# Kernel tuning notes

Measured on AMD Instinct MI355X. Metric: run time of the kernel, lower is better.

## Reference

```python
import jax, jax.numpy as jnp
import numpy as np


def _pair_indices(field_num):
    # upper-triangular (row < col) pairs, same order as the torch double loop
    r, c = np.triu_indices(field_num, k=1)
    return jnp.asarray(r, dtype=jnp.int32), jnp.asarray(c, dtype=jnp.int32)


def setup_inputs() -> dict:
    key = jax.random.key(0)
    x = jax.random.normal(key, (4096, 39, 64), dtype=jnp.float32)
    return {"x": x}


def reference(x) -> jnp.ndarray:
    # x: (B, F, D). Output: (B, F*(F-1)/2) pairwise inner products.
    field_num = x.shape[1]
    rows, cols = _pair_indices(field_num)  # static: derived from shape
    p = x[:, rows, :]  # (B, P, D) gather of row-field embeddings
    q = x[:, cols, :]  # (B, P, D) gather of col-field embeddings
    return jnp.sum(p * q, axis=2)  # (B, P)
```

## Files before the change

kernel.cpp:

```cpp
#include <hip/hip_runtime.h>


constexpr int NFIELD = 39;
constexpr int DIM    = 64;
constexpr int K4     = DIM / 4;
constexpr int NPAIR  = 741;
constexpr int NROWP  = 40;
constexpr int BPB    = 4;
constexpr int NB     = 10;
constexpr int NTILE  = NB * (NB + 1) / 2;
constexpr int F4B    = NFIELD * K4;

__global__ __launch_bounds__(256)
void ip_kernel(const float4* __restrict__ x4, float* __restrict__ out, int batches) {
    __shared__ float4 lds[BPB][NROWP][K4];
    __shared__ __align__(16) float lds_out[BPB][NPAIR];

    const int tid = threadIdx.x;
    const int b0  = blockIdx.x * BPB;
    const int nb_here = (batches - b0) < BPB ? (batches - b0) : BPB;

    const int n4 = nb_here * F4B;
    const float4* src = x4 + (size_t)b0 * F4B;
    for (int idx = tid; idx < n4; idx += 256) {
        int bl  = idx / F4B;
        int rem = idx - bl * F4B;
        int row = rem >> 4;
        int k   = rem & 15;
        lds[bl][row][(k + (row >> 2)) & 15] = src[idx];
    }
    __syncthreads();

    const int lane  = tid & 63;
    const int wv    = tid >> 6;
    const int batch = b0 + wv;

    if (batch < batches && lane < NTILE) {
        int bi = 0, rem = lane;
        while (rem >= NB - bi) { rem -= NB - bi; ++bi; }
        const int bj = bi + rem;

        const int ra = bi * 4, rb = bj * 4;
        float acc[4][4];
        #pragma unroll
        for (int a = 0; a < 4; ++a)
            #pragma unroll
            for (int b = 0; b < 4; ++b) acc[a][b] = 0.0f;

        #pragma unroll 2
        for (int k = 0; k < K4; ++k) {
            const int ka = (k + bi) & 15;
            const int kb = (k + bj) & 15;
            float4 av[4];
            #pragma unroll
            for (int ii = 0; ii < 4; ++ii) av[ii] = lds[wv][ra + ii][ka];
            #pragma unroll
            for (int jj = 0; jj < 4; ++jj) {
                const float4 bv = lds[wv][rb + jj][kb];
                #pragma unroll
                for (int ii = 0; ii < 4; ++ii) {
                    acc[ii][jj] = fmaf(av[ii].x, bv.x, acc[ii][jj]);
                    acc[ii][jj] = fmaf(av[ii].y, bv.y, acc[ii][jj]);
                    acc[ii][jj] = fmaf(av[ii].z, bv.z, acc[ii][jj]);
                    acc[ii][jj] = fmaf(av[ii].w, bv.w, acc[ii][jj]);
                }
            }
        }

        #pragma unroll
        for (int ii = 0; ii < 4; ++ii) {
            const int i = ra + ii;
            #pragma unroll
            for (int jj = 0; jj < 4; ++jj) {
                const int j = rb + jj;
                if (j < NFIELD && i < j) {
                    const int p = 38 * i - (i * (i - 1)) / 2 + (j - i - 1);
                    lds_out[wv][p] = acc[ii][jj];
                }
            }
        }
    }
    __syncthreads();

    float* dst = out + (size_t)b0 * NPAIR;
    const float* srcf = &lds_out[0][0];
    if (nb_here == BPB) {
        const float4* s4 = (const float4*)srcf;
        float4* d4 = (float4*)dst;
        for (int i = tid; i < (BPB * NPAIR) / 4; i += 256) d4[i] = s4[i];
    } else {
        const int nfl = nb_here * NPAIR;
        for (int i = tid; i < nfl; i += 256) dst[i] = srcf[i];
    }
}

extern "C" void kernel_launch(void* const* d_in, const int* in_sizes, int n_in,
                              void* d_out, int out_size, void* d_ws, size_t ws_size,
                              hipStream_t stream) {
    const float* x = (const float*)d_in[0];
    float* out     = (float*)d_out;
    const int batches = in_sizes[0] / (NFIELD * DIM);
    const int blocks  = (batches + BPB - 1) / BPB;
    ip_kernel<<<blocks, 256, 0, stream>>>((const float4*)x, out, batches);
}
```

Before: 86.11 us.

## Compute pairwise inner products with bf16 MFMA on swizzled LDS tiles

Converts the fp32 embeddings to bf16 while staging them in LDS, using an XOR-swizzled layout padded to 48 rows. Each wave then computes the upper-triangular 16x16 tiles of the 39x39 Gram matrix with mfma_f32_16x16x32_bf16 instead of scalar FMAs. This removes most of the ALU and LDS-read work of the fp32 register-tiled loop. The cost is reduced input precision (bf16), which may exceed the reference tolerance, and the kernel is likely dominated by memory traffic anyway.

```diff
diff --git a/kernel.cpp b/kernel.cpp
--- a/kernel.cpp
+++ b/kernel.cpp
@@ -1,84 +1,88 @@
 #include <hip/hip_runtime.h>
 
 
+typedef __bf16 bf16x8 __attribute__((ext_vector_type(8)));
+typedef float  f32x4  __attribute__((ext_vector_type(4)));
+
 constexpr int NFIELD = 39;
 constexpr int DIM    = 64;
-constexpr int K4     = DIM / 4;
 constexpr int NPAIR  = 741;
-constexpr int NROWP  = 40;
 constexpr int BPB    = 4;
-constexpr int NB     = 10;
-constexpr int NTILE  = NB * (NB + 1) / 2;
-constexpr int F4B    = NFIELD * K4;
+constexpr int NROWS  = 48;
+constexpr int CPR    = 8;
+constexpr int CPB    = NFIELD * CPR;
 
 __global__ __launch_bounds__(256)
 void ip_kernel(const float4* __restrict__ x4, float* __restrict__ out, int batches) {
-    __shared__ float4 lds[BPB][NROWP][K4];
-    __shared__ __align__(16) float lds_out[BPB][NPAIR];
+    __shared__ __align__(16) __bf16 xs[BPB][NROWS][DIM];
+    __shared__ __align__(16) float  lds_out[BPB][NPAIR];
 
     const int tid = threadIdx.x;
     const int b0  = blockIdx.x * BPB;
     const int nb_here = (batches - b0) < BPB ? (batches - b0) : BPB;
 
-    const int n4 = nb_here * F4B;
-    const float4* src = x4 + (size_t)b0 * F4B;
-    for (int idx = tid; idx < n4; idx += 256) {
-        int bl  = idx / F4B;
-        int rem = idx - bl * F4B;
-        int row = rem >> 4;
-        int k   = rem & 15;
-        lds[bl][row][(k + (row >> 2)) & 15] = src[idx];
+    for (int c = tid; c < nb_here * 9 * CPR; c += 256) {
+        int bl  = c / (9 * CPR);
+        int rem = c - bl * (9 * CPR);
+        int row = NFIELD + (rem >> 3);
+        int ch  = rem & 7;
+        int4 z; z.x = 0; z.y = 0; z.z = 0; z.w = 0;
+        *(int4*)&xs[bl][row][(ch ^ (row & 7)) * 8] = z;
+    }
+
+    const float4* src = x4 + (size_t)b0 * (CPB * 2);
+    for (int c = tid; c < nb_here * CPB; c += 256) {
+        float4 u = src[2 * c];
+        float4 v = src[2 * c + 1];
+        int bl  = c / CPB;
+        int rem = c - bl * CPB;
+        int row = rem >> 3;
+        int ch  = rem & 7;
+        bf16x8 w;
+        w[0] = (__bf16)u.x; w[1] = (__bf16)u.y; w[2] = (__bf16)u.z; w[3] = (__bf16)u.w;
+        w[4] = (__bf16)v.x; w[5] = (__bf16)v.y; w[6] = (__bf16)v.z; w[7] = (__bf16)v.w;
+        *(bf16x8*)&xs[bl][row][(ch ^ (row & 7)) * 8] = w;
     }
     __syncthreads();
 
+    const int wv    = tid >> 6;
     const int lane  = tid & 63;
-    const int wv    = tid >> 6;
     const int batch = b0 + wv;
 
-    if (batch < batches && lane < NTILE) {
-        int bi = 0, rem = lane;
-        while (rem >= NB - bi) { rem -= NB - bi; ++bi; }
-        const int bj = bi + rem;
+    if (batch < batches) {
+        const int m = lane & 15;
+        const int q = lane >> 4;
 
-        const int ra = bi * 4, rb = bj * 4;
-        float acc[4][4];
+        f32x4 a00 = {0.f,0.f,0.f,0.f}, a01 = a00, a02 = a00;
+        f32x4 a11 = a00, a12 = a00, a22 = a00;
+
         #pragma unroll
-        for (int a = 0; a < 4; ++a)
+        for (int s = 0; s < 2; ++s) {
+            const int pc = ((4 * s + q) ^ (m & 7)) * 8;
+            bf16x8 f0 = *(const bf16x8*)&xs[wv][ 0 + m][pc];
+            bf16x8 f1 = *(const bf16x8*)&xs[wv][16 + m][pc];
+            bf16x8 f2 = *(const bf16x8*)&xs[wv][32 + m][pc];
+            a00 = __builtin_amdgcn_mfma_f32_16x16x32_bf16(f0, f0, a00, 0, 0, 0);
+            a01 = __builtin_amdgcn_mfma_f32_16x16x32_bf16(f0, f1, a01, 0, 0, 0);
+            a02 = __builtin_amdgcn_mfma_f32_16x16x32_bf16(f0, f2, a02, 0, 0, 0);
+            a11 = __builtin_amdgcn_mfma_f32_16x16x32_bf16(f1, f1, a11, 0, 0, 0);
+            a12 = __builtin_amdgcn_mfma_f32_16x16x32_bf16(f1, f2, a12, 0, 0, 0);
+            a22 = __builtin_amdgcn_mfma_f32_16x16x32_bf16(f2, f2, a22, 0, 0, 0);
+        }
+
+        auto scatter = [&](const f32x4& a, int ti, int tj) {
             #pragma unroll
-            for (int b = 0; b < 4; ++b) acc[a][b] = 0.0f;
-
-        #pragma unroll 2
-        for (int k = 0; k < K4; ++k) {
-            const int ka = (k + bi) & 15;
-            const int kb = (k + bj) & 15;
-            float4 av[4];
-            #pragma unroll
-            for (int ii = 0; ii < 4; ++ii) av[ii] = lds[wv][ra + ii][ka];
-            #pragma unroll
-            for (int jj = 0; jj < 4; ++jj) {
-                const float4 bv = lds[wv][rb + jj][kb];
-                #pragma unroll
-                for (int ii = 0; ii < 4; ++ii) {
-                    acc[ii][jj] = fmaf(av[ii].x, bv.x, acc[ii][jj]);
-                    acc[ii][jj] = fmaf(av[ii].y, bv.y, acc[ii][jj]);
-                    acc[ii][jj] = fmaf(av[ii].z, bv.z, acc[ii][jj]);
-                    acc[ii][jj] = fmaf(av[ii].w, bv.w, acc[ii][jj]);
+            for (int r = 0; r < 4; ++r) {
+                const int i = 16 * ti + 4 * q + r;
+                const int j = 16 * tj + m;
+                if (i < j && j < NFIELD) {
+                    const int p = 38 * i - (i * (i - 1)) / 2 + (j - i - 1);
+                    lds_out[wv][p] = a[r];
                 }
             }
-        }
-
-        #pragma unroll
-        for (int ii = 0; ii < 4; ++ii) {
-            const int i = ra + ii;
-            #pragma unroll
-            for (int jj = 0; jj < 4; ++jj) {
-                const int j = rb + jj;
-                if (j < NFIELD && i < j) {
-                    const int p = 38 * i - (i * (i - 1)) / 2 + (j - i - 1);
-                    lds_out[wv][p] = acc[ii][jj];
-                }
-            }
-        }
+        };
+        scatter(a00, 0, 0); scatter(a01, 0, 1); scatter(a02, 0, 2);
+        scatter(a11, 1, 1); scatter(a12, 1, 2); scatter(a22, 2, 2);
     }
     __syncthreads();
 
```

Result: faster. 79.40 us (-7.8%).
